# Optimization experiments

Measured on AMD Instinct MI355X. Metric: run time of the kernel, lower is better.

The kernel has to match this reference:

```python
import jax, jax.numpy as jnp
import numpy as np
from jax import lax

B, CIN, H, W = 32, 256, 28, 28
COUT, KS, KEXP = 256, 3, 4
HIDDEN = int(CIN * 0.25)  # ratio hard-coded to 0.25 in the module


def setup_inputs() -> dict:
    key = jax.random.key(0)
    k1, k2, k3, k4 = jax.random.split(key, 4)
    x = jax.random.normal(k1, (B, CIN, H, W), dtype=jnp.float32)
    # SE (InvertedEx) params: fc1 (1x1 conv, no bias), fc2 (1x1 conv, bias)
    fc1_w = jax.random.normal(k2, (HIDDEN, CIN), dtype=jnp.float32) * np.float32(np.sqrt(2.0 / CIN))
    fc2_w = jax.random.normal(k3, (KEXP * COUT, HIDDEN), dtype=jnp.float32) * np.float32(np.sqrt(2.0 / HIDDEN))
    fc2_b = jnp.zeros((KEXP * COUT,), dtype=jnp.float32)
    # K expert conv kernels, he_std = sqrt(2) * (CIN*KS^2)^-0.5
    he_std = np.float32(np.sqrt(2.0) * (CIN * KS * KS) ** -0.5)
    weight = jax.random.normal(k4, (KEXP, COUT, CIN, KS, KS), dtype=jnp.float32) * he_std
    return {"x": x, "fc1_w": fc1_w, "fc2_w": fc2_w, "fc2_b": fc2_b, "weight": weight}


def reference(x, fc1_w, fc2_w, fc2_b, weight):
    # --- SE routing ---
    pooled = jnp.mean(x, axis=(2, 3))                        # [B, CIN]
    h = jax.nn.relu(pooled @ fc1_w.T)                        # [B, HIDDEN]
    y = (h @ fc2_w.T + fc2_b).reshape(B, KEXP, COUT)         # [B, K, COUT]
    prob = jax.nn.softmax(y / jnp.sqrt(jnp.float32(HIDDEN)), axis=1)  # softmax over K
    # --- aggregate per-sample kernels ---
    agg_w = jnp.einsum('bko,koihw->boihw', prob, weight)     # [B, COUT, CIN, KS, KS]
    # --- per-sample conv (batched implicit GEMM via vmap) ---
    def conv1(xi, wi):
        return lax.conv_general_dilated(
            xi[None], wi, window_strides=(1, 1), padding=((1, 1), (1, 1)),
            dimension_numbers=('NCHW', 'OIHW', 'NCHW'))[0]
    out = jax.vmap(conv1)(x, agg_w)                          # [B, COUT, H, W]
    return out
```

## Files before the change

### kernel.cpp

```cpp
#include <hip/hip_runtime.h>
#include <math.h>

#define B_    32
#define CIN_  256
#define HW_   784
#define H_    28
#define W_    28
#define COUT_ 256
#define KEXP_ 4
#define HID_  64

typedef short short8 __attribute__((ext_vector_type(8)));
typedef unsigned short ushort4v __attribute__((ext_vector_type(4)));
typedef unsigned short ushort8v __attribute__((ext_vector_type(8)));
typedef float floatx16 __attribute__((ext_vector_type(16)));
typedef float float8v __attribute__((ext_vector_type(8)));

__device__ __forceinline__ unsigned short f2bf(float f) {
    union { float f; unsigned int u; } v; v.f = f;
    unsigned int r = (v.u + 0x7FFFu + ((v.u >> 16) & 1u)) >> 16;
    return (unsigned short)r;
}

__global__ __launch_bounds__(256) void xpose_pool_kernel(const float* __restrict__ x,
                                                         unsigned short* __restrict__ x_t,
                                                         float* __restrict__ partial) {
    __shared__ float tile[32][33];
    int bid = blockIdx.x;
    int b   = bid / 200;
    int rem = bid - b * 200;
    int icg = rem / 25;
    int pxt = rem % 25;
    int ic0 = icg * 32;
    int px0 = pxt * 32;
    int t = threadIdx.x;
    int c = t & 31, rr = t >> 5;
    #pragma unroll
    for (int r = 0; r < 4; ++r) {
        int icr = rr + r * 8;
        int px = px0 + c;
        float v = (px < HW_) ? x[((size_t)(b * CIN_ + ic0 + icr)) * HW_ + px] : 0.f;
        tile[icr][c] = v;
    }
    __syncthreads();
    #pragma unroll
    for (int r = 0; r < 4; ++r) {
        int pxr = rr + r * 8;
        int px = px0 + pxr;
        if (px < HW_)
            x_t[((size_t)b * HW_ + px) * CIN_ + ic0 + c] = f2bf(tile[c][pxr]);
    }
    if (t < 32) {
        float s = 0.f;
        #pragma unroll
        for (int cc = 0; cc < 32; ++cc) s += tile[t][cc];
        partial[((size_t)b * 25 + pxt) * CIN_ + ic0 + t] = s * (1.0f / HW_);
    }
}

__global__ __launch_bounds__(256) void pool_kernel(const float* __restrict__ x,
                                                   float* __restrict__ pooled) {
    int w = blockIdx.x * 4 + (threadIdx.x >> 6);
    int lane = threadIdx.x & 63;
    const float* p = x + (size_t)w * HW_;
    float s = 0.f;
    for (int i = lane; i < HW_; i += 64) s += p[i];
    for (int off = 32; off; off >>= 1) s += __shfl_down(s, off);
    if (lane == 0) pooled[w] = s * (1.0f / HW_);
}

__global__ __launch_bounds__(256) void se3_kernel(const float* __restrict__ partial,
                                                  const float* __restrict__ fc1_w,
                                                  const float* __restrict__ fc2_w,
                                                  const float* __restrict__ fc2_b,
                                                  float* __restrict__ prob) {
    __shared__ float pl[CIN_];
    __shared__ float h[HID_];
    __shared__ float wb[16640];
    int b = blockIdx.x, t = threadIdx.x;
    {
        float s = 0.f;
        for (int pt = 0; pt < 25; ++pt)
            s += partial[((size_t)b * 25 + pt) * CIN_ + t];
        pl[t] = s;
    }
    #pragma unroll
    for (int i = 0; i < 16; ++i) {
        int l = t + i * 256;
        float4 v = *(const float4*)(fc1_w + (size_t)l * 4);
        int r = l >> 6, cc = (l & 63) * 4;
        float* dst = &wb[r * 257 + cc];
        dst[0] = v.x; dst[1] = v.y; dst[2] = v.z; dst[3] = v.w;
    }
    __syncthreads();
    if (t < HID_) {
        float s = 0.f;
        const float* wr = &wb[t * 257];
        for (int c = 0; c < CIN_; ++c) s += pl[c] * wr[c];
        h[t] = fmaxf(s, 0.f);
    }
    float yk[KEXP_];
    for (int k = 0; k < KEXP_; ++k) {
        __syncthreads();
        #pragma unroll
        for (int i = 0; i < 16; ++i) {
            int l = t + i * 256;
            float4 v = *(const float4*)(fc2_w + (size_t)k * COUT_ * HID_ + (size_t)l * 4);
            int o = l >> 4, jj = (l & 15) * 4;
            float* dst = &wb[o * 65 + jj];
            dst[0] = v.x; dst[1] = v.y; dst[2] = v.z; dst[3] = v.w;
        }
        __syncthreads();
        float s = fc2_b[k * COUT_ + t];
        const float* wr = &wb[t * 65];
        #pragma unroll
        for (int j = 0; j < HID_; ++j) s += h[j] * wr[j];
        yk[k] = s * 0.125f;
    }
    float m = yk[0];
    for (int k = 1; k < KEXP_; ++k) m = fmaxf(m, yk[k]);
    float e[KEXP_], sum = 0.f;
    for (int k = 0; k < KEXP_; ++k) { e[k] = expf(yk[k] - m); sum += e[k]; }
    float inv = 1.0f / sum;
    for (int k = 0; k < KEXP_; ++k)
        prob[b * (KEXP_ * COUT_) + k * COUT_ + t] = e[k] * inv;
}

__global__ __launch_bounds__(256) void se2_kernel(const float* __restrict__ pooled,
                                                  const float* __restrict__ fc1_w,
                                                  const float* __restrict__ fc2_w,
                                                  const float* __restrict__ fc2_b,
                                                  float* __restrict__ prob) {
    __shared__ float pl[CIN_];
    __shared__ float h[HID_];
    __shared__ float wb[16640];
    int b = blockIdx.x, t = threadIdx.x;
    pl[t] = pooled[b * CIN_ + t];
    #pragma unroll
    for (int i = 0; i < 16; ++i) {
        int l = t + i * 256;
        float4 v = *(const float4*)(fc1_w + (size_t)l * 4);
        int r = l >> 6, cc = (l & 63) * 4;
        float* dst = &wb[r * 257 + cc];
        dst[0] = v.x; dst[1] = v.y; dst[2] = v.z; dst[3] = v.w;
    }
    __syncthreads();
    if (t < HID_) {
        float s = 0.f;
        const float* wr = &wb[t * 257];
        for (int c = 0; c < CIN_; ++c) s += pl[c] * wr[c];
        h[t] = fmaxf(s, 0.f);
    }
    float yk[KEXP_];
    for (int k = 0; k < KEXP_; ++k) {
        __syncthreads();
        #pragma unroll
        for (int i = 0; i < 16; ++i) {
            int l = t + i * 256;
            float4 v = *(const float4*)(fc2_w + (size_t)k * COUT_ * HID_ + (size_t)l * 4);
            int o = l >> 4, jj = (l & 15) * 4;
            float* dst = &wb[o * 65 + jj];
            dst[0] = v.x; dst[1] = v.y; dst[2] = v.z; dst[3] = v.w;
        }
        __syncthreads();
        float s = fc2_b[k * COUT_ + t];
        const float* wr = &wb[t * 65];
        #pragma unroll
        for (int j = 0; j < HID_; ++j) s += h[j] * wr[j];
        yk[k] = s * 0.125f;
    }
    float m = yk[0];
    for (int k = 1; k < KEXP_; ++k) m = fmaxf(m, yk[k]);
    float e[KEXP_], sum = 0.f;
    for (int k = 0; k < KEXP_; ++k) { e[k] = expf(yk[k] - m); sum += e[k]; }
    float inv = 1.0f / sum;
    for (int k = 0; k < KEXP_; ++k)
        prob[b * (KEXP_ * COUT_) + k * COUT_ + t] = e[k] * inv;
}

__global__ __launch_bounds__(256) void agg4_kernel(const float* __restrict__ weight,
                                                   const float* __restrict__ prob,
                                                   unsigned short* __restrict__ agg) {
    __shared__ float wlds[4][32][145];
    int gid = blockIdx.x;
    int og  = gid & 7;
    int icc = (gid >> 3) & 3;
    int kk  = (gid >> 5) & 3;
    int bh  = gid >> 7;
    int oc0 = og * 32;
    int ic0 = icc * 64 + kk * 16;
    int t = threadIdx.x;

    #pragma unroll
    for (int i = 0; i < 18; ++i) {
        int idx = t + i * 256;
        int k  = idx / 1152;
        int r  = idx - k * 1152;
        int oc = r / 36;
        int f4 = r - oc * 36;
        float4 v = *(const float4*)(weight + ((size_t)(k * COUT_ + oc0 + oc) * CIN_ + ic0) * 9 + f4 * 4);
        float* dst = &wlds[k][oc][f4 * 4];
        dst[0] = v.x; dst[1] = v.y; dst[2] = v.z; dst[3] = v.w;
    }

    int lane = t & 63, wv = t >> 6;
    int ml = lane & 31, kh = lane >> 5;

    float pbr[4][4];
    #pragma unroll
    for (int bi = 0; bi < 4; ++bi) {
        int b = bh * 16 + wv * 4 + bi;
        #pragma unroll
        for (int k = 0; k < 4; ++k)
            pbr[bi][k] = prob[(size_t)b * (KEXP_ * COUT_) + k * COUT_ + oc0 + ml];
    }
    __syncthreads();

    for (int rs = 0; rs < 9; ++rs) {
        float wreg[4][8];
        #pragma unroll
        for (int k = 0; k < 4; ++k)
            #pragma unroll
            for (int j = 0; j < 8; ++j)
                wreg[k][j] = wlds[k][ml][(kh * 8 + j) * 9 + rs];
        #pragma unroll
        for (int bi = 0; bi < 4; ++bi) {
            int b = bh * 16 + wv * 4 + bi;
            ushort8v pack;
            #pragma unroll
            for (int j = 0; j < 8; ++j) {
                float s = pbr[bi][0] * wreg[0][j] + pbr[bi][1] * wreg[1][j]
                        + pbr[bi][2] * wreg[2][j] + pbr[bi][3] * wreg[3][j];
                pack[j] = f2bf(s);
            }
            *(ushort8v*)(agg + (size_t)(b * 16 + icc * 4 + kk) * 36864
                             + (size_t)rs * 4096 + og * 512 + lane * 8) = pack;
        }
    }
}

__global__ __launch_bounds__(256, 2) void conv_mfma6_kernel(const unsigned short* __restrict__ x_t,
                                                            const unsigned short* __restrict__ agg,
                                                            float* __restrict__ out) {
    __shared__ __align__(16) short Xs[2][6 * 35 * 72];

    int gid = blockIdx.x;
    int b      = gid & 31;
    int half   = (gid >> 5) & 1;
    int oc0    = half * 128;
    int rowblk = gid >> 6;
    int py0 = rowblk * 4;

    int t = threadIdx.x;
    int lane = t & 63, w = t >> 6;
    int ml = lane & 31, kh = lane >> 5;
    int og = half * 4 + w;

    floatx16 acc[4];
    #pragma unroll
    for (int j = 0; j < 4; ++j)
        #pragma unroll
        for (int r = 0; r < 16; ++r) acc[j][r] = 0.f;

    const unsigned short* xtb = x_t + (size_t)b * HW_ * CIN_;
    const unsigned short* aln = agg + (size_t)b * 589824 + og * 512 + lane * 8;

    short8 Abuf[4][3];
    #pragma unroll
    for (int s = 0; s < 3; ++s) {
        #pragma unroll
        for (int tap = 0; tap < 3; ++tap)
            Abuf[s][tap] = *(const short8*)(aln + (size_t)(s / 3) * 36864
                                                + (size_t)(s % 3) * 4096
                                                + (size_t)tap * 12288);
    }

    {
        #pragma unroll
        for (int i = 0; i < 7; ++i) {
            int l = t + i * 256;
            if (l < 1680) {
                int pos = l >> 3, g = l & 7;
                int row = pos / 35, col = pos - row * 35;
                int gy = py0 - 1 + row, gx = col - 1;
                short8 v = (short8)0;
                if ((unsigned)gy < 28u && (unsigned)gx < 28u)
                    v = *(const short8*)(xtb + ((size_t)(gy * W_ + gx)) * CIN_ + g * 8);
                *(short8*)&Xs[0][pos * 72 + g * 8] = v;
            }
        }
    }

    __syncthreads();

    #pragma unroll
    for (int c = 0; c < 4; ++c) {
        const short* xb = &Xs[c & 1][0];

        short8 Xl[7];
        if (c < 3) {
            #pragma unroll
            for (int i = 0; i < 7; ++i) {
                int l = t + i * 256;
                short8 v = (short8)0;
                if (l < 1680) {
                    int pos = l >> 3, g = l & 7;
                    int row = pos / 35, col = pos - row * 35;
                    int gy = py0 - 1 + row, gx = col - 1;
                    if ((unsigned)gy < 28u && (unsigned)gx < 28u)
                        v = *(const short8*)(xtb + ((size_t)(gy * W_ + gx)) * CIN_ + c * 64 + 64 + g * 8);
                }
                Xl[i] = v;
            }
        }

        #pragma unroll
        for (int s = 0; s < 12; ++s) {
            const int g  = c * 12 + s;
            const int gp = g + 3;
            if (gp < 48) {
                const int cc  = gp / 12;
                const int kkp = (gp % 12) / 3;
                const int dxp = gp % 3;
                const unsigned short* ap = aln + (size_t)cc * 147456
                                               + (size_t)kkp * 36864 + (size_t)dxp * 4096;
                #pragma unroll
                for (int tap = 0; tap < 3; ++tap)
                    Abuf[gp & 3][tap] = *(const short8*)(ap + (size_t)tap * 12288);
            }
            const int kk = s / 3, dx = s % 3;
            const int sl = g & 3;
            int va = (ml + dx) * 72 + kk * 16 + kh * 8;
            #pragma unroll
            for (int r = 0; r < 6; ++r) {
                short8 Bf = *(const short8*)&xb[r * 2520 + va];
                if (r <= 3)
                    acc[r]     = __builtin_amdgcn_mfma_f32_32x32x16_bf16(Abuf[sl][0], Bf, acc[r], 0, 0, 0);
                if (r >= 1 && r - 1 <= 3)
                    acc[r - 1] = __builtin_amdgcn_mfma_f32_32x32x16_bf16(Abuf[sl][1], Bf, acc[r - 1], 0, 0, 0);
                if (r >= 2)
                    acc[r - 2] = __builtin_amdgcn_mfma_f32_32x32x16_bf16(Abuf[sl][2], Bf, acc[r - 2], 0, 0, 0);
            }
        }

        if (c < 3) {
            short* dstb = &Xs[(c & 1) ^ 1][0];
            #pragma unroll
            for (int i = 0; i < 7; ++i) {
                int l = t + i * 256;
                if (l < 1680) {
                    int pos = l >> 3, g = l & 7;
                    *(short8*)&dstb[pos * 72 + g * 8] = Xl[i];
                }
            }
        }
        __syncthreads();
    }

    if (ml < W_) {
        #pragma unroll
        for (int j = 0; j < 4; ++j) {
            float* op = out + ((size_t)(b * COUT_ + oc0 + w * 32)) * HW_ + (py0 + j) * W_ + ml;
            #pragma unroll
            for (int r = 0; r < 16; ++r) {
                int ocd = (r & 3) + 8 * (r >> 2) + 4 * kh;
                op[(size_t)ocd * HW_] = acc[j][r];
            }
        }
    }
}

__global__ __launch_bounds__(256) void conv_kernel(const float* __restrict__ x,
                                                   const float* __restrict__ weight,
                                                   const float* __restrict__ prob,
                                                   float* __restrict__ out) {
    __shared__ float xs[30 * 30];
    __shared__ float wagg[8][32][12];
    __shared__ float pl[KEXP_][8];

    int b  = blockIdx.x >> 5;
    int o0 = (blockIdx.x & 31) * 8;
    int t  = threadIdx.x;

    if (t < 32) {
        int k = t >> 3, oc = t & 7;
        pl[k][oc] = prob[b * (KEXP_ * COUT_) + k * COUT_ + o0 + oc];
    }
    int p0 = t;
    int pr[4], pc[4];
    bool pv[4];
    #pragma unroll
    for (int j = 0; j < 4; ++j) {
        int p = p0 + j * 256;
        pv[j] = p < HW_;
        pr[j] = p / W_;
        pc[j] = p % W_;
    }
    float acc[8][4];
    #pragma unroll
    for (int oc = 0; oc < 8; ++oc)
        #pragma unroll
        for (int j = 0; j < 4; ++j) acc[oc][j] = 0.f;

    int aoc = t >> 5, aii = t & 31;

    for (int ic0 = 0; ic0 < CIN_; ic0 += 32) {
        __syncthreads();
        {
            float w9[9];
            #pragma unroll
            for (int j = 0; j < 9; ++j) w9[j] = 0.f;
            int i = ic0 + aii;
            #pragma unroll
            for (int k = 0; k < KEXP_; ++k) {
                float pk = pl[k][aoc];
                const float* wp = weight + ((size_t)(k * COUT_ + o0 + aoc) * CIN_ + i) * 9;
                #pragma unroll
                for (int j = 0; j < 9; ++j) w9[j] += pk * wp[j];
            }
            #pragma unroll
            for (int j = 0; j < 9; ++j) wagg[aoc][aii][j] = w9[j];
        }
        for (int ii = 0; ii < 32; ++ii) {
            int i = ic0 + ii;
            __syncthreads();
            const float* xp = x + (size_t)(b * CIN_ + i) * HW_;
            for (int e = t; e < 900; e += 256) {
                int ry = e / 30, cx = e - ry * 30;
                int gy = ry - 1, gx = cx - 1;
                float v = 0.f;
                if ((unsigned)gy < 28u && (unsigned)gx < 28u) v = xp[gy * W_ + gx];
                xs[e] = v;
            }
            __syncthreads();
            float xv[4][9];
            #pragma unroll
            for (int j = 0; j < 4; ++j) {
                if (pv[j]) {
                    const float* xr = &xs[pr[j] * 30 + pc[j]];
                    xv[j][0] = xr[0];  xv[j][1] = xr[1];  xv[j][2] = xr[2];
                    xv[j][3] = xr[30]; xv[j][4] = xr[31]; xv[j][5] = xr[32];
                    xv[j][6] = xr[60]; xv[j][7] = xr[61]; xv[j][8] = xr[62];
                } else {
                    #pragma unroll
                    for (int q = 0; q < 9; ++q) xv[j][q] = 0.f;
                }
            }
            #pragma unroll
            for (int oc = 0; oc < 8; ++oc) {
                float4 wa = *(const float4*)&wagg[oc][ii][0];
                float4 wb2 = *(const float4*)&wagg[oc][ii][4];
                float  wc = wagg[oc][ii][8];
                #pragma unroll
                for (int j = 0; j < 4; ++j) {
                    acc[oc][j] += xv[j][0] * wa.x + xv[j][1] * wa.y + xv[j][2] * wa.z
                                + xv[j][3] * wa.w + xv[j][4] * wb2.x + xv[j][5] * wb2.y
                                + xv[j][6] * wb2.z + xv[j][7] * wb2.w + xv[j][8] * wc;
                }
            }
        }
    }
    #pragma unroll
    for (int oc = 0; oc < 8; ++oc) {
        float* op = out + (size_t)(b * COUT_ + o0 + oc) * HW_ + p0;
        #pragma unroll
        for (int j = 0; j < 4; ++j)
            if (pv[j]) op[j * 256] = acc[oc][j];
    }
}

extern "C" void kernel_launch(void* const* d_in, const int* in_sizes, int n_in,
                              void* d_out, int out_size, void* d_ws, size_t ws_size,
                              hipStream_t stream) {
    const float* x     = (const float*)d_in[0];
    const float* fc1_w = (const float*)d_in[1];
    const float* fc2_w = (const float*)d_in[2];
    const float* fc2_b = (const float*)d_in[3];
    const float* weight= (const float*)d_in[4];
    float* out = (float*)d_out;

    char* ws = (char*)d_ws;
    float* prob = (float*)(ws);
    unsigned short* x_t = (unsigned short*)(ws + 131072);
    unsigned short* agg = (unsigned short*)(ws + 12976128);
    float* partial = (float*)(ws + 12976128);
    const size_t WS_NEED = 12976128 + (size_t)B_ * 9 * COUT_ * CIN_ * 2;

    if (ws_size >= WS_NEED) {
        xpose_pool_kernel<<<B_ * 8 * 25, 256, 0, stream>>>(x, x_t, partial);
        se3_kernel<<<B_, 256, 0, stream>>>(partial, fc1_w, fc2_w, fc2_b, prob);
        agg4_kernel<<<256, 256, 0, stream>>>(weight, prob, agg);
        conv_mfma6_kernel<<<448, 256, 0, stream>>>(x_t, agg, out);
    } else {
        float* pooled = (float*)(ws + 131072);
        pool_kernel<<<(B_ * CIN_) / 4, 256, 0, stream>>>(x, pooled);
        se2_kernel<<<B_, 256, 0, stream>>>(pooled, fc1_w, fc2_w, fc2_b, prob);
        conv_kernel<<<B_ * (COUT_ / 8), 256, 0, stream>>>(x, weight, prob, out);
    }
}
```

Measured before the change: 148.0 us.

## Stage conv operands via direct global-to-LDS loads with swizzled LDS layout

The MFMA conv kernel now streams both the activation halo tile and the aggregated weight fragments into LDS using global_load_lds DMA, replacing register-staged copies. Padding reads point at a zeroed scratch buffer written by the transpose kernel, and the channel chunks shrink from 64 to 32 with an XOR-swizzled LDS layout to avoid bank conflicts. Explicit vmcnt waits and scheduling barriers build a deeper software pipeline. This aims to cut VGPR pressure and load latency, at the cost of fragile hand-tuned wait counts and more barriers.

```diff
diff --git a/kernel.cpp b/kernel.cpp
--- a/kernel.cpp
+++ b/kernel.cpp
@@ -14,7 +14,15 @@
 typedef unsigned short ushort4v __attribute__((ext_vector_type(4)));
 typedef unsigned short ushort8v __attribute__((ext_vector_type(8)));
 typedef float floatx16 __attribute__((ext_vector_type(16)));
-typedef float float8v __attribute__((ext_vector_type(8)));
+
+#define AS1 __attribute__((address_space(1)))
+#define AS3 __attribute__((address_space(3)))
+__device__ __forceinline__ void glds16(const void* g, void* l) {
+    __builtin_amdgcn_global_load_lds((const AS1 unsigned int*)g,
+                                     (AS3 unsigned int*)l, 16, 0, 0);
+}
+#define VMW(N) asm volatile("s_waitcnt vmcnt(" #N ")" ::: "memory")
+#define SB()   __builtin_amdgcn_sched_barrier(0)
 
 __device__ __forceinline__ unsigned short f2bf(float f) {
     union { float f; unsigned int u; } v; v.f = f;
@@ -24,7 +32,8 @@
 
 __global__ __launch_bounds__(256) void xpose_pool_kernel(const float* __restrict__ x,
                                                          unsigned short* __restrict__ x_t,
-                                                         float* __restrict__ partial) {
+                                                         float* __restrict__ partial,
+                                                         float* __restrict__ zp) {
     __shared__ float tile[32][33];
     int bid = blockIdx.x;
     int b   = bid / 200;
@@ -34,6 +43,10 @@
     int ic0 = icg * 32;
     int px0 = pxt * 32;
     int t = threadIdx.x;
+    if (bid == 0 && t == 0) {
+        float4 z; z.x = 0.f; z.y = 0.f; z.z = 0.f; z.w = 0.f;
+        *(float4*)zp = z;
+    }
     int c = t & 31, rr = t >> 5;
     #pragma unroll
     for (int r = 0; r < 4; ++r) {
@@ -239,10 +252,12 @@
     }
 }
 
-__global__ __launch_bounds__(256, 2) void conv_mfma6_kernel(const unsigned short* __restrict__ x_t,
+__global__ __launch_bounds__(256, 2) void conv_mfma8_kernel(const unsigned short* __restrict__ x_t,
                                                             const unsigned short* __restrict__ agg,
+                                                            const float* __restrict__ zp,
                                                             float* __restrict__ out) {
-    __shared__ __align__(16) short Xs[2][6 * 35 * 72];
+    __shared__ __align__(16) short Xs[2][6720];
+    __shared__ __align__(16) short Alds[24576];
 
     int gid = blockIdx.x;
     int b      = gid & 31;
@@ -255,6 +270,7 @@
     int lane = t & 63, w = t >> 6;
     int ml = lane & 31, kh = lane >> 5;
     int og = half * 4 + w;
+    int kh16 = kh << 4;
 
     floatx16 acc[4];
     #pragma unroll
@@ -263,98 +279,108 @@
         for (int r = 0; r < 16; ++r) acc[j][r] = 0.f;
 
     const unsigned short* xtb = x_t + (size_t)b * HW_ * CIN_;
-    const unsigned short* aln = agg + (size_t)b * 589824 + og * 512 + lane * 8;
-
-    short8 Abuf[4][3];
-    #pragma unroll
-    for (int s = 0; s < 3; ++s) {
-        #pragma unroll
-        for (int tap = 0; tap < 3; ++tap)
-            Abuf[s][tap] = *(const short8*)(aln + (size_t)(s / 3) * 36864
-                                                + (size_t)(s % 3) * 4096
-                                                + (size_t)tap * 12288);
-    }
-
-    {
-        #pragma unroll
-        for (int i = 0; i < 7; ++i) {
+    const unsigned short* ag  = agg + (size_t)b * 589824 + og * 512 + lane * 8;
+
+    int off[3][6];
+    #pragma unroll
+    for (int dx = 0; dx < 3; ++dx)
+        #pragma unroll
+        for (int r = 0; r < 6; ++r) {
+            int a = ml + dx + 35 * r;
+            off[dx][r] = a * 64 + ((((a & 3) ^ ((a >> 2) & 1))) << 4);
+        }
+
+    auto stageXs = [&](int cc, int bb) {
+        #pragma unroll
+        for (int i = 0; i < 3; ++i) {
             int l = t + i * 256;
-            if (l < 1680) {
-                int pos = l >> 3, g = l & 7;
-                int row = pos / 35, col = pos - row * 35;
-                int gy = py0 - 1 + row, gx = col - 1;
-                short8 v = (short8)0;
-                if ((unsigned)gy < 28u && (unsigned)gx < 28u)
-                    v = *(const short8*)(xtb + ((size_t)(gy * W_ + gx)) * CIN_ + g * 8);
-                *(short8*)&Xs[0][pos * 72 + g * 8] = v;
-            }
-        }
-    }
-
-    __syncthreads();
-
-    #pragma unroll
-    for (int c = 0; c < 4; ++c) {
-        const short* xb = &Xs[c & 1][0];
-
-        short8 Xl[7];
-        if (c < 3) {
-            #pragma unroll
-            for (int i = 0; i < 7; ++i) {
-                int l = t + i * 256;
-                short8 v = (short8)0;
-                if (l < 1680) {
-                    int pos = l >> 3, g = l & 7;
-                    int row = pos / 35, col = pos - row * 35;
-                    int gy = py0 - 1 + row, gx = col - 1;
-                    if ((unsigned)gy < 28u && (unsigned)gx < 28u)
-                        v = *(const short8*)(xtb + ((size_t)(gy * W_ + gx)) * CIN_ + c * 64 + 64 + g * 8);
-                }
-                Xl[i] = v;
-            }
-        }
-
-        #pragma unroll
-        for (int s = 0; s < 12; ++s) {
-            const int g  = c * 12 + s;
-            const int gp = g + 3;
-            if (gp < 48) {
-                const int cc  = gp / 12;
-                const int kkp = (gp % 12) / 3;
-                const int dxp = gp % 3;
-                const unsigned short* ap = aln + (size_t)cc * 147456
-                                               + (size_t)kkp * 36864 + (size_t)dxp * 4096;
-                #pragma unroll
-                for (int tap = 0; tap < 3; ++tap)
-                    Abuf[gp & 3][tap] = *(const short8*)(ap + (size_t)tap * 12288);
-            }
-            const int kk = s / 3, dx = s % 3;
-            const int sl = g & 3;
-            int va = (ml + dx) * 72 + kk * 16 + kh * 8;
-            #pragma unroll
-            for (int r = 0; r < 6; ++r) {
-                short8 Bf = *(const short8*)&xb[r * 2520 + va];
-                if (r <= 3)
-                    acc[r]     = __builtin_amdgcn_mfma_f32_32x32x16_bf16(Abuf[sl][0], Bf, acc[r], 0, 0, 0);
-                if (r >= 1 && r - 1 <= 3)
-                    acc[r - 1] = __builtin_amdgcn_mfma_f32_32x32x16_bf16(Abuf[sl][1], Bf, acc[r - 1], 0, 0, 0);
-                if (r >= 2)
-                    acc[r - 2] = __builtin_amdgcn_mfma_f32_32x32x16_bf16(Abuf[sl][2], Bf, acc[r - 2], 0, 0, 0);
-            }
-        }
-
-        if (c < 3) {
-            short* dstb = &Xs[(c & 1) ^ 1][0];
-            #pragma unroll
-            for (int i = 0; i < 7; ++i) {
-                int l = t + i * 256;
-                if (l < 1680) {
-                    int pos = l >> 3, g = l & 7;
-                    *(short8*)&dstb[pos * 72 + g * 8] = Xl[i];
-                }
-            }
-        }
-        __syncthreads();
+            int pos = l >> 2, gl = l & 3;
+            int g8 = gl ^ (pos & 3) ^ ((pos >> 2) & 1);
+            int row = pos / 35, col = pos - row * 35;
+            int gy = py0 - 1 + row, gx = col - 1;
+            const void* src = ((unsigned)gy < 28u && (unsigned)gx < 28u)
+                ? (const void*)(xtb + ((size_t)(gy * W_ + gx)) * CIN_ + cc * 32 + g8 * 8)
+                : (const void*)zp;
+            glds16(src, &Xs[bb][(w * 64 + i * 256) * 8]);
+        }
+        if (w < 2) {
+            int l = t + 768;
+            int pos = l >> 2, gl = l & 3;
+            int g8 = gl ^ (pos & 3) ^ ((pos >> 2) & 1);
+            int row = pos / 35, col = pos - row * 35;
+            int gy = py0 - 1 + row, gx = col - 1;
+            const void* src = (l < 840 && (unsigned)gy < 28u && (unsigned)gx < 28u)
+                ? (const void*)(xtb + ((size_t)(gy * W_ + gx)) * CIN_ + cc * 32 + g8 * 8)
+                : (const void*)zp;
+            if (l < 840)
+                glds16(src, &Xs[bb][(w * 64 + 768) * 8]);
+        }
+    };
+
+    auto dmaA = [&](int gg) {
+        int c3  = gg / 6;
+        int icc = c3 >> 1;
+        int kk4 = (c3 & 1) * 2 + (gg % 6) / 3;
+        int dx3 = gg % 3;
+        const unsigned short* sp = ag + icc * 147456 + kk4 * 36864 + dx3 * 4096;
+        short* d = &Alds[((w * 4 + (gg & 3)) * 3) * 512];
+        glds16(sp,         d);
+        glds16(sp + 12288, d + 512);
+        glds16(sp + 24576, d + 1024);
+    };
+
+    stageXs(0, 0);  SB();
+    dmaA(0);        SB();
+    dmaA(1);        SB();
+    dmaA(2);        SB();
+    VMW(6);         SB();
+    __builtin_amdgcn_s_barrier();
+
+    short8 Areg[2][3];
+    #pragma unroll
+    for (int tap = 0; tap < 3; ++tap)
+        Areg[0][tap] = *(const short8*)&Alds[((w * 4 + 0) * 3 + tap) * 512 + lane * 8];
+
+    #pragma unroll
+    for (int g = 0; g < 48; ++g) {
+        const int c  = g / 6;
+        const int s  = g % 6;
+        const int kk = s / 3;
+        const int dx = g % 3;
+
+        if (g + 3 < 48)      { dmaA(g + 3);                  SB(); }
+        if (s == 3 && c < 7) { stageXs(c + 1, (c + 1) & 1);  SB(); }
+
+        if (g == 45)      { VMW(3); }
+        else if (g == 46) { VMW(0); }
+        else if (g < 45 && s >= 3 && c < 7) { VMW(9); }
+        else if (g < 47)  { VMW(6); }
+        SB();
+
+        if (g < 47) {
+            #pragma unroll
+            for (int tap = 0; tap < 3; ++tap)
+                Areg[(g + 1) & 1][tap] =
+                    *(const short8*)&Alds[((w * 4 + ((g + 1) & 3)) * 3 + tap) * 512 + lane * 8];
+        }
+
+        const char* xbc = (const char*)&Xs[c & 1][0];
+        const int kxor = (kk << 5) | kh16;
+        #pragma unroll
+        for (int r = 0; r < 6; ++r) {
+            short8 Bf = *(const short8*)(xbc + (off[dx][r] ^ kxor));
+            if (r <= 3)
+                acc[r]     = __builtin_amdgcn_mfma_f32_32x32x16_bf16(Areg[g & 1][0], Bf, acc[r], 0, 0, 0);
+            if (r >= 1 && r <= 4)
+                acc[r - 1] = __builtin_amdgcn_mfma_f32_32x32x16_bf16(Areg[g & 1][1], Bf, acc[r - 1], 0, 0, 0);
+            if (r >= 2)
+                acc[r - 2] = __builtin_amdgcn_mfma_f32_32x32x16_bf16(Areg[g & 1][2], Bf, acc[r - 2], 0, 0, 0);
+        }
+
+        if (s == 5 && c < 7) {
+            VMW(6);  SB();
+            __builtin_amdgcn_s_barrier();
+        }
     }
 
     if (ml < W_) {
@@ -484,13 +510,14 @@
     unsigned short* x_t = (unsigned short*)(ws + 131072);
     unsigned short* agg = (unsigned short*)(ws + 12976128);
     float* partial = (float*)(ws + 12976128);
-    const size_t WS_NEED = 12976128 + (size_t)B_ * 9 * COUT_ * CIN_ * 2;
+    float* zp   = (float*)(ws + 50724864);
+    const size_t WS_NEED = 50724864 + 4096;
 
     if (ws_size >= WS_NEED) {
-        xpose_pool_kernel<<<B_ * 8 * 25, 256, 0, stream>>>(x, x_t, partial);
+        xpose_pool_kernel<<<B_ * 8 * 25, 256, 0, stream>>>(x, x_t, partial, zp);
         se3_kernel<<<B_, 256, 0, stream>>>(partial, fc1_w, fc2_w, fc2_b, prob);
         agg4_kernel<<<256, 256, 0, stream>>>(weight, prob, agg);
-        conv_mfma6_kernel<<<448, 256, 0, stream>>>(x_t, agg, out);
+        conv_mfma8_kernel<<<448, 256, 0, stream>>>(x_t, agg, zp, out);
     } else {
         float* pooled = (float*)(ws + 131072);
         pool_kernel<<<(B_ * CIN_) / 4, 256, 0, stream>>>(x, pooled);
```

Measured after the change: 145.3 us. About the same (-1.8%).

## Double output channels per wave to reuse LDS input tile, halving grid

Applied to the files above, without the earlier changes.

Each wave now computes two 32-channel output tiles (64 channels) instead of one, so a block covers all 256 output channels and the grid shrinks from 448 to 224 blocks. Every B fragment read from LDS now feeds twice as many MFMAs, and each input tile is staged once per block rather than once per channel half. Sched barriers are added around the weight and input prefetch loads to control instruction ordering. In exchange register pressure roughly doubles (launch bounds drop to one block per SM) and 224 blocks may underfill the device, costing occupancy and latency hiding.

```diff
diff --git a/kernel.cpp b/kernel.cpp
--- a/kernel.cpp
+++ b/kernel.cpp
@@ -14,7 +14,8 @@
 typedef unsigned short ushort4v __attribute__((ext_vector_type(4)));
 typedef unsigned short ushort8v __attribute__((ext_vector_type(8)));
 typedef float floatx16 __attribute__((ext_vector_type(16)));
-typedef float float8v __attribute__((ext_vector_type(8)));
+
+#define SB() __builtin_amdgcn_sched_barrier(0)
 
 __device__ __forceinline__ unsigned short f2bf(float f) {
     union { float f; unsigned int u; } v; v.f = f;
@@ -239,41 +240,42 @@
     }
 }
 
-__global__ __launch_bounds__(256, 2) void conv_mfma6_kernel(const unsigned short* __restrict__ x_t,
-                                                            const unsigned short* __restrict__ agg,
-                                                            float* __restrict__ out) {
+__global__ __launch_bounds__(256, 1) void conv_mfma10_kernel(const unsigned short* __restrict__ x_t,
+                                                             const unsigned short* __restrict__ agg,
+                                                             float* __restrict__ out) {
     __shared__ __align__(16) short Xs[2][6 * 35 * 72];
 
     int gid = blockIdx.x;
     int b      = gid & 31;
-    int half   = (gid >> 5) & 1;
-    int oc0    = half * 128;
-    int rowblk = gid >> 6;
+    int rowblk = gid >> 5;
     int py0 = rowblk * 4;
 
     int t = threadIdx.x;
     int lane = t & 63, w = t >> 6;
     int ml = lane & 31, kh = lane >> 5;
-    int og = half * 4 + w;
-
-    floatx16 acc[4];
-    #pragma unroll
-    for (int j = 0; j < 4; ++j)
-        #pragma unroll
-        for (int r = 0; r < 16; ++r) acc[j][r] = 0.f;
+
+    floatx16 acc[2][4];
+    #pragma unroll
+    for (int u = 0; u < 2; ++u)
+        #pragma unroll
+        for (int j = 0; j < 4; ++j)
+            #pragma unroll
+            for (int r = 0; r < 16; ++r) acc[u][j][r] = 0.f;
 
     const unsigned short* xtb = x_t + (size_t)b * HW_ * CIN_;
-    const unsigned short* aln = agg + (size_t)b * 589824 + og * 512 + lane * 8;
-
-    short8 Abuf[4][3];
+    const unsigned short* aln0 = agg + (size_t)b * 589824 + (w * 2 + 0) * 512 + lane * 8;
+    const unsigned short* aln1 = agg + (size_t)b * 589824 + (w * 2 + 1) * 512 + lane * 8;
+
+    short8 Abuf[4][2][3];
     #pragma unroll
     for (int s = 0; s < 3; ++s) {
         #pragma unroll
-        for (int tap = 0; tap < 3; ++tap)
-            Abuf[s][tap] = *(const short8*)(aln + (size_t)(s / 3) * 36864
-                                                + (size_t)(s % 3) * 4096
-                                                + (size_t)tap * 12288);
-    }
+        for (int tap = 0; tap < 3; ++tap) {
+            Abuf[s][0][tap] = *(const short8*)(aln0 + (size_t)s * 4096 + (size_t)tap * 12288);
+            Abuf[s][1][tap] = *(const short8*)(aln1 + (size_t)s * 4096 + (size_t)tap * 12288);
+        }
+    }
+    SB();
 
     {
         #pragma unroll
@@ -312,6 +314,7 @@
                 }
                 Xl[i] = v;
             }
+            SB();
         }
 
         #pragma unroll
@@ -322,11 +325,13 @@
                 const int cc  = gp / 12;
                 const int kkp = (gp % 12) / 3;
                 const int dxp = gp % 3;
-                const unsigned short* ap = aln + (size_t)cc * 147456
-                                               + (size_t)kkp * 36864 + (size_t)dxp * 4096;
+                const size_t po = (size_t)cc * 147456 + (size_t)kkp * 36864 + (size_t)dxp * 4096;
                 #pragma unroll
-                for (int tap = 0; tap < 3; ++tap)
-                    Abuf[gp & 3][tap] = *(const short8*)(ap + (size_t)tap * 12288);
+                for (int tap = 0; tap < 3; ++tap) {
+                    Abuf[gp & 3][0][tap] = *(const short8*)(aln0 + po + (size_t)tap * 12288);
+                    Abuf[gp & 3][1][tap] = *(const short8*)(aln1 + po + (size_t)tap * 12288);
+                }
+                SB();
             }
             const int kk = s / 3, dx = s % 3;
             const int sl = g & 3;
@@ -334,12 +339,15 @@
             #pragma unroll
             for (int r = 0; r < 6; ++r) {
                 short8 Bf = *(const short8*)&xb[r * 2520 + va];
-                if (r <= 3)
-                    acc[r]     = __builtin_amdgcn_mfma_f32_32x32x16_bf16(Abuf[sl][0], Bf, acc[r], 0, 0, 0);
-                if (r >= 1 && r - 1 <= 3)
-                    acc[r - 1] = __builtin_amdgcn_mfma_f32_32x32x16_bf16(Abuf[sl][1], Bf, acc[r - 1], 0, 0, 0);
-                if (r >= 2)
-                    acc[r - 2] = __builtin_amdgcn_mfma_f32_32x32x16_bf16(Abuf[sl][2], Bf, acc[r - 2], 0, 0, 0);
+                #pragma unroll
+                for (int u = 0; u < 2; ++u) {
+                    if (r <= 3)
+                        acc[u][r]     = __builtin_amdgcn_mfma_f32_32x32x16_bf16(Abuf[sl][u][0], Bf, acc[u][r], 0, 0, 0);
+                    if (r >= 1 && r <= 4)
+                        acc[u][r - 1] = __builtin_amdgcn_mfma_f32_32x32x16_bf16(Abuf[sl][u][1], Bf, acc[u][r - 1], 0, 0, 0);
+                    if (r >= 2)
+                        acc[u][r - 2] = __builtin_amdgcn_mfma_f32_32x32x16_bf16(Abuf[sl][u][2], Bf, acc[u][r - 2], 0, 0, 0);
+                }
             }
         }
 
@@ -359,12 +367,15 @@
 
     if (ml < W_) {
         #pragma unroll
-        for (int j = 0; j < 4; ++j) {
-            float* op = out + ((size_t)(b * COUT_ + oc0 + w * 32)) * HW_ + (py0 + j) * W_ + ml;
-            #pragma unroll
-            for (int r = 0; r < 16; ++r) {
-                int ocd = (r & 3) + 8 * (r >> 2) + 4 * kh;
-                op[(size_t)ocd * HW_] = acc[j][r];
+        for (int u = 0; u < 2; ++u) {
+            #pragma unroll
+            for (int j = 0; j < 4; ++j) {
+                float* op = out + ((size_t)(b * COUT_ + w * 64 + u * 32)) * HW_ + (py0 + j) * W_ + ml;
+                #pragma unroll
+                for (int r = 0; r < 16; ++r) {
+                    int ocd = (r & 3) + 8 * (r >> 2) + 4 * kh;
+                    op[(size_t)ocd * HW_] = acc[u][j][r];
+                }
             }
         }
     }
@@ -490,7 +501,7 @@
         xpose_pool_kernel<<<B_ * 8 * 25, 256, 0, stream>>>(x, x_t, partial);
         se3_kernel<<<B_, 256, 0, stream>>>(partial, fc1_w, fc2_w, fc2_b, prob);
         agg4_kernel<<<256, 256, 0, stream>>>(weight, prob, agg);
-        conv_mfma6_kernel<<<448, 256, 0, stream>>>(x_t, agg, out);
+        conv_mfma10_kernel<<<224, 256, 0, stream>>>(x_t, agg, out);
     } else {
         float* pooled = (float*)(ws + 131072);
         pool_kernel<<<(B_ * CIN_) / 4, 256, 0, stream>>>(x, pooled);
```

New measurement: 145.0 us, median of 2. -2.0%, faster.
